# Optimization experiments

Hardware: AMD Instinct MI355X
Metric: run time of the kernel (lower is better)

Reference implementation:

```python
import jax, jax.numpy as jnp
import numpy as np

EPS = 1e-5


def _conv1x1(x, w, b):
    # x: (B,C,H,W), w: (O,C), b: (O,)
    return jnp.einsum('oc,bchw->bohw', w, x) + b[None, :, None, None]


def _attn(q, k, v):
    # q,k: (B,Dq,H,W); v: (B,C,H,W). Full NxN attention, softmax over keys.
    B, _, H, W = q.shape
    N = H * W
    Q = q.reshape(B, -1, N)
    K = k.reshape(B, -1, N)
    V = v.reshape(B, -1, N)
    A = jax.nn.softmax(jnp.einsum('bci,bcj->bij', Q, K), axis=-1)  # (B,N,N)
    out = jnp.einsum('bcj,bij->bci', V, A)  # out[b,c,i] = sum_j V[b,c,j] A[b,i,j]
    return out.reshape(B, -1, H, W)


def _std(feat):
    # torch.var(dim=2) is unbiased (ddof=1)
    B, C = feat.shape[:2]
    v = jnp.var(feat.reshape(B, C, -1), axis=2, ddof=1) + EPS
    return jnp.sqrt(v)[:, :, None, None]


def _fmm(fb_feat, bg_feat):
    return fb_feat * (_std(bg_feat) / _std(fb_feat))


def setup_inputs() -> dict:
    key = jax.random.key(0)
    ks = jax.random.split(key, 16)
    B, C, H, W = 2, 256, 64, 64
    D = C // 8
    s = 0.05
    inp = {
        'x': jax.random.normal(ks[0], (B, C, H, W), jnp.float32),
        'mask': jax.random.randint(ks[1], (B, 1, H, W), 0, 2).astype(jnp.float32),
        'sa_wq': jax.random.normal(ks[2], (D, C), jnp.float32) * s,
        'sa_bq': jax.random.normal(ks[3], (D,), jnp.float32) * s,
        'sa_wk': jax.random.normal(ks[4], (D, C), jnp.float32) * s,
        'sa_bk': jax.random.normal(ks[5], (D,), jnp.float32) * s,
        'sa_wv': jax.random.normal(ks[6], (C, C), jnp.float32) * s,
        'sa_bv': jax.random.normal(ks[7], (C,), jnp.float32) * s,
        'sa_gamma': jax.random.uniform(ks[8], (1,), jnp.float32),
        'wq': jax.random.normal(ks[9], (D, C), jnp.float32) * s,
        'bq': jax.random.normal(ks[10], (D,), jnp.float32) * s,
        'wk': jax.random.normal(ks[11], (D, C), jnp.float32) * s,
        'bk': jax.random.normal(ks[12], (D,), jnp.float32) * s,
        'wv': jax.random.normal(ks[13], (C, C), jnp.float32) * s,
        'bv': jax.random.normal(ks[14], (C,), jnp.float32) * s,
        'gamma': jax.random.uniform(ks[15], (1,), jnp.float32),
    }
    return inp


def reference(x, mask, sa_wq, sa_bq, sa_wk, sa_bk, sa_wv, sa_bv, sa_gamma,
              wq, bq, wk, bk, wv, bv, gamma):
    # --- Self_Attn ---
    sa_out = _attn(_conv1x1(x, sa_wq, sa_bq),
                   _conv1x1(x, sa_wk, sa_bk),
                   _conv1x1(x, sa_wv, sa_bv))
    x = sa_gamma[0] * sa_out + x
    # --- FB_FMM masked cross attention (mask already at feature resolution) ---
    reverse_mask = 1.0 - mask
    feature_b = reverse_mask * x
    feature_f = mask * x
    sw_bg = _attn(_conv1x1(feature_f, wq, bq),
                  _conv1x1(feature_b, wk, bk),
                  _conv1x1(feature_b, wv, bv))
    out = x + gamma[0] * _fmm(feature_f, sw_bg)
    return out
```

## Files before the change

### kernel.cpp

```cpp
#include <hip/hip_runtime.h>
#include <stdint.h>

typedef _Float16 f16;
typedef __attribute__((ext_vector_type(8))) _Float16 half8;
typedef __attribute__((ext_vector_type(2))) __fp16 fp16x2;
typedef __attribute__((ext_vector_type(8))) short short8;
typedef __attribute__((ext_vector_type(4))) float f32x4;

#define NPOS 4096
#define CCH  256
#define OQK  64
#define BATCH 2
#define NSPLIT 4
#define KEYS_PER_SPLIT 1024
#define NT (KEYS_PER_SPLIT / 64)

typedef __attribute__((address_space(3))) uint32_t lds_u32;
typedef __attribute__((address_space(1))) const uint32_t glb_u32;

__device__ __forceinline__ float bf2f(short u) {
    union { uint32_t i; float f; } c;
    c.i = ((uint32_t)(uint16_t)u) << 16;
    return c.f;
}
__device__ __forceinline__ short f2bf(float f) {
    union { float f; uint32_t i; } c; c.f = f;
    uint32_t lsb = (c.i >> 16) & 1u;
    c.i += 0x7FFFu + lsb;
    return (short)(c.i >> 16);
}

__device__ __forceinline__ bool detect_bf16(const uint32_t* mw) {
    int hits = 0;
    #pragma unroll
    for (int i = 0; i < 64; ++i) hits += ((mw[i] & 0xFFFFu) == 0x3F80u) ? 1 : 0;
    return hits != 0;
}

__device__ __forceinline__ void load8(const void* base, size_t e0, bool bf, float* v) {
    if (bf) {
        short8 s = *(const short8*)((const short*)base + e0);
        #pragma unroll
        for (int j = 0; j < 8; ++j) v[j] = bf2f(s[j]);
    } else {
        const float* fp = (const float*)base + e0;
        float4 a = *(const float4*)fp;
        float4 b = *(const float4*)(fp + 4);
        v[0] = a.x; v[1] = a.y; v[2] = a.z; v[3] = a.w;
        v[4] = b.x; v[5] = b.y; v[6] = b.z; v[7] = b.w;
    }
}
__device__ __forceinline__ float load1(const void* base, int i, bool bf) {
    return bf ? bf2f(((const short*)base)[i]) : ((const float*)base)[i];
}

__device__ __forceinline__ int pkrtz(float a, float b) {
    union { fp16x2 h; int i; } u;
    u.h = __builtin_amdgcn_cvt_pkrtz(a, b);
    return u.i;
}

__global__ __launch_bounds__(256) void convert_inputs(
    const uint32_t* __restrict__ mask_raw,
    const void* __restrict__ w1q, const void* __restrict__ w1k, const void* __restrict__ w1v_,
    const void* __restrict__ b1q, const void* __restrict__ b1k, const void* __restrict__ b1v_,
    const void* __restrict__ g1,
    const void* __restrict__ w2q, const void* __restrict__ w2k, const void* __restrict__ w2v_,
    const void* __restrict__ b2q, const void* __restrict__ b2k, const void* __restrict__ b2v_,
    const void* __restrict__ g2,
    float* __restrict__ maskf,
    f16* __restrict__ w1qk, f16* __restrict__ w1vm, f16* __restrict__ b1,
    f16* __restrict__ w2qk, f16* __restrict__ w2vm, f16* __restrict__ b2,
    float* __restrict__ gam)
{
    const bool bf = detect_bf16(mask_raw);
    const int blk = blockIdx.x, tid = threadIdx.x;
    float v[8];
    if (blk < 4) {
        const size_t e0 = ((size_t)blk * 256 + tid) * 8;
        load8(mask_raw, e0, bf, v);
        float4 f0 = {v[0], v[1], v[2], v[3]}, f1 = {v[4], v[5], v[6], v[7]};
        *(float4*)(maskf + e0) = f0;
        *(float4*)(maskf + e0 + 4) = f1;
    } else if (blk < 12) {
        const size_t g = ((size_t)(blk - 4) * 256 + tid) * 8;
        const int o = (int)(g >> 8), cc = (int)(g & 255);
        const void* src = (o < 32) ? w1q : w1k;
        const size_t se = (size_t)((o < 32) ? o : o - 32) * 256 + cc;
        load8(src, se, bf, v);
        half8 h;
        #pragma unroll
        for (int j = 0; j < 8; ++j) h[j] = (f16)v[j];
        *(half8*)(w1qk + g) = h;
    } else if (blk < 44) {
        const size_t g = ((size_t)(blk - 12) * 256 + tid) * 8;
        load8(w1v_, g, bf, v);
        half8 h;
        #pragma unroll
        for (int j = 0; j < 8; ++j) h[j] = (f16)v[j];
        *(half8*)(w1vm + g) = h;
    } else if (blk < 52) {
        const size_t g = ((size_t)(blk - 44) * 256 + tid) * 8;
        const int o = (int)(g >> 8), cc = (int)(g & 255);
        const void* src = (o < 32) ? w2q : w2k;
        const size_t se = (size_t)((o < 32) ? o : o - 32) * 256 + cc;
        load8(src, se, bf, v);
        half8 h;
        #pragma unroll
        for (int j = 0; j < 8; ++j) h[j] = (f16)v[j];
        *(half8*)(w2qk + g) = h;
    } else if (blk < 84) {
        const size_t g = ((size_t)(blk - 52) * 256 + tid) * 8;
        load8(w2v_, g, bf, v);
        half8 h;
        #pragma unroll
        for (int j = 0; j < 8; ++j) h[j] = (f16)v[j];
        *(half8*)(w2vm + g) = h;
    } else {
        for (int i = tid; i < 320; i += 256) {
            const void* s1 = (i < 32) ? b1q : (i < 64) ? b1k : b1v_;
            const void* s2 = (i < 32) ? b2q : (i < 64) ? b2k : b2v_;
            const int ii = (i < 32) ? i : (i < 64) ? i - 32 : i - 64;
            b1[i] = (f16)load1(s1, ii, bf);
            b2[i] = (f16)load1(s2, ii, bf);
        }
        if (tid == 0) {
            gam[0] = load1(g1, 0, bf);
            gam[1] = load1(g2, 0, bf);
        }
    }
}

__global__ __launch_bounds__(256) void conv_qkv(
    const void* __restrict__ xin, int is_raw,
    const uint32_t* __restrict__ mask_raw,
    const f16* __restrict__ wqk,
    const f16* __restrict__ wvm,
    const f16* __restrict__ bias,
    const float* __restrict__ maskf, int use_mask,
    f16* __restrict__ qkout,
    f16* __restrict__ vout)
{
    const bool bf = is_raw ? detect_bf16(mask_raw) : false;
    const int b    = blockIdx.y;
    const int n0   = blockIdx.x * 32;
    const int tid  = threadIdx.x;
    const int lane = tid & 63;
    const int w    = tid >> 6;
    const int lo   = lane & 15;
    const int hi   = lane >> 4;

    __shared__ f16 xt[32 * 256];

    {
        const int nc = tid & 3;
        const int cg = tid >> 2;
        #pragma unroll
        for (int it = 0; it < 4; ++it) {
            const int c = cg + 64 * it;
            const size_t off = ((size_t)b * CCH + c) * NPOS + n0 + nc * 8;
            float v8[8];
            load8(xin, off, bf, v8);
            #pragma unroll
            for (int j = 0; j < 8; ++j) {
                const int n = nc * 8 + j;
                int byte = n * 512 + c * 2;
                byte ^= ((n & 7) << 4);
                *(f16*)((char*)xt + byte) = (f16)v8[j];
            }
        }
    }
    __syncthreads();

    const f32x4 z = {0.f, 0.f, 0.f, 0.f};
    f32x4 acc_qk[2];
    f32x4 acc_v[4][2];
    #pragma unroll
    for (int i = 0; i < 2; ++i) {
        acc_qk[i] = z;
        #pragma unroll
        for (int j = 0; j < 4; ++j) acc_v[j][i] = z;
    }

    #pragma unroll 1
    for (int ks = 0; ks < 8; ++ks) {
        const int ce = ks * 32 + 8 * hi;
        half8 xfr[2];
        #pragma unroll
        for (int nt = 0; nt < 2; ++nt) {
            const int n = nt * 16 + lo;
            int byte = n * 512 + ce * 2;
            byte ^= ((n & 7) << 4);
            xfr[nt] = *(const half8*)((const char*)xt + byte);
        }
        {
            half8 wf = *(const half8*)(wqk + (size_t)(w * 16 + lo) * 256 + ce);
            #pragma unroll
            for (int nt = 0; nt < 2; ++nt)
                acc_qk[nt] = __builtin_amdgcn_mfma_f32_16x16x32_f16(xfr[nt], wf, acc_qk[nt], 0, 0, 0);
        }
        #pragma unroll
        for (int ot = 0; ot < 4; ++ot) {
            half8 wf = *(const half8*)(wvm + (size_t)(w * 64 + ot * 16 + lo) * 256 + ce);
            #pragma unroll
            for (int nt = 0; nt < 2; ++nt)
                acc_v[ot][nt] = __builtin_amdgcn_mfma_f32_16x16x32_f16(wf, xfr[nt], acc_v[ot][nt], 0, 0, 0);
        }
    }

    {
        const int o = w * 16 + lo;
        const float bb = (float)bias[o];
        #pragma unroll
        for (int nt = 0; nt < 2; ++nt) {
            #pragma unroll
            for (int r = 0; r < 4; ++r) {
                const int n = n0 + nt * 16 + 4 * hi + r;
                float mult = 1.f;
                if (use_mask) {
                    const float mv = maskf[b * NPOS + n];
                    mult = (o < 32) ? mv : (1.f - mv);
                }
                qkout[((size_t)b * NPOS + n) * OQK + o] = (f16)(mult * acc_qk[nt][r] + bb);
            }
        }
    }
    {
        float mv_n[2];
        #pragma unroll
        for (int nt = 0; nt < 2; ++nt)
            mv_n[nt] = use_mask ? (1.f - maskf[b * NPOS + n0 + nt * 16 + lo]) : 1.f;
        #pragma unroll
        for (int ot = 0; ot < 4; ++ot) {
            #pragma unroll
            for (int r = 0; r < 4; ++r) {
                const int oc = w * 64 + ot * 16 + 4 * hi + r;
                const float bb = (float)bias[64 + oc];
                #pragma unroll
                for (int nt = 0; nt < 2; ++nt) {
                    const int n = n0 + nt * 16 + lo;
                    vout[((size_t)b * CCH + oc) * NPOS + n] = (f16)(mv_n[nt] * acc_v[ot][nt][r] + bb);
                }
            }
        }
    }
}

__global__ __launch_bounds__(256, 2) void attn_split(
    const f16* __restrict__ qk,
    const f16* __restrict__ vbuf,
    f16* __restrict__ po,
    float2* __restrict__ pml)
{
    const int b     = blockIdx.z;
    const int split = blockIdx.y;
    const int tid   = threadIdx.x;
    const int lane  = tid & 63;
    const int w     = tid >> 6;
    const int lo    = lane & 15;
    const int hi    = lane >> 4;
    const int q0    = blockIdx.x * 64;
    const int qown  = w * 16;
    const int qA    = (w >> 1) * 32;
    const int qB    = qA + 16;
    const int cbase = (w & 1) * 128;

    __shared__ f16 kv[CCH * 64];
    __shared__ f16 kbuf[2][64 * 64];
    __shared__ f16 plds[64 * 72];
    __shared__ float sc_lds[64];
    __shared__ float l_lds[64];
    __shared__ int   flag_lds[4];

    const int trow = tid >> 3;
    const int tch  = tid & 7;

    const half8 qfrag = *(const half8*)(qk + ((size_t)b * NPOS + q0 + qown + lo) * OQK + 8 * hi);

    const f32x4 z = {0.f, 0.f, 0.f, 0.f};
    f32x4 accA[8], accB[8];
    #pragma unroll
    for (int i = 0; i < 8; ++i) { accA[i] = z; accB[i] = z; }
    float m_run = -3.0e38f, l_run = 0.f;

    const f16* vsrc = vbuf + (size_t)b * CCH * NPOS;
    const f16* ksrc = qk + (size_t)b * NPOS * OQK;

    #define STAGE_K(kt)                                                        \
    {                                                                          \
        const int j0s = split * KEYS_PER_SPLIT + (kt) * 64;                    \
        char* kb = (char*)kbuf + ((kt) & 1) * 8192;                            \
        _Pragma("unroll")                                                      \
        for (int i = 0; i < 2; ++i) {                                          \
            const int j = i * 32 + trow;                                       \
            const f16* g = ksrc + (size_t)(j0s + j) * OQK + ((tch ^ (j & 7)) * 8); \
            char* d = kb + i * 4096 + w * 1024;                                \
            __builtin_amdgcn_global_load_lds((glb_u32*)g, (lds_u32*)d, 16, 0, 0); \
        }                                                                      \
    }
    #define STAGE_V(kt)                                                        \
    {                                                                          \
        const int j0s = split * KEYS_PER_SPLIT + (kt) * 64;                    \
        _Pragma("unroll")                                                      \
        for (int i = 0; i < 8; ++i) {                                          \
            const int c = i * 32 + trow;                                       \
            const f16* g = vsrc + (size_t)c * NPOS + j0s + ((tch ^ (c & 7)) * 8); \
            char* d = (char*)kv + i * 4096 + w * 1024;                         \
            __builtin_amdgcn_global_load_lds((glb_u32*)g, (lds_u32*)d, 16, 0, 0); \
        }                                                                      \
    }

    STAGE_K(0)
    STAGE_V(0)

    #pragma unroll 1
    for (int kt = 0; kt < NT; ++kt) {
        asm volatile("s_waitcnt vmcnt(8)" ::: "memory");
        __builtin_amdgcn_s_barrier();
        asm volatile("" ::: "memory");
        if (kt + 1 < NT) STAGE_K(kt + 1)

        const char* kb = (const char*)kbuf + (kt & 1) * 8192;
        f32x4 s[4];
        __builtin_amdgcn_s_setprio(1);
        #pragma unroll
        for (int jt = 0; jt < 4; ++jt) {
            const int krow = jt * 16 + lo;
            const half8 kfrag = *(const half8*)(kb + krow * 128
                                                + ((64 + hi * 16) ^ ((krow & 7) << 4)));
            s[jt] = __builtin_amdgcn_mfma_f32_16x16x32_f16(kfrag, qfrag, z, 0, 0, 0);
        }
        __builtin_amdgcn_s_setprio(0);
        float pm = s[0][0];
        #pragma unroll
        for (int jt = 0; jt < 4; ++jt)
            #pragma unroll
            for (int r = 0; r < 4; ++r) pm = fmaxf(pm, s[jt][r]);
        pm = fmaxf(pm, __shfl_xor(pm, 16, 64));
        pm = fmaxf(pm, __shfl_xor(pm, 32, 64));
        const bool g = __any(pm - m_run > 8.f);
        float scv = 1.f;
        if (g) {
            const float mnew = fmaxf(m_run, pm);
            scv = __expf(m_run - mnew);
            m_run = mnew;
            l_run *= scv;
        }
        float rs = 0.f;
        #pragma unroll
        for (int jt = 0; jt < 4; ++jt) {
            #pragma unroll
            for (int r = 0; r < 4; ++r) {
                const float pv = __expf(s[jt][r] - m_run);
                s[jt][r] = pv;
                rs += pv;
            }
        }
        rs += __shfl_xor(rs, 16, 64);
        rs += __shfl_xor(rs, 32, 64);
        l_run += rs;
        #pragma unroll
        for (int jt = 0; jt < 4; ++jt) {
            union { int i2[2]; uint64_t u; } pw;
            pw.i2[0] = pkrtz(s[jt][0], s[jt][1]);
            pw.i2[1] = pkrtz(s[jt][2], s[jt][3]);
            *(uint64_t*)((char*)plds + (qown + lo) * 144 + jt * 32 + 8 * hi) = pw.u;
        }
        if (hi == 0) sc_lds[qown + lo] = scv;
        if (lane == 0) flag_lds[w] = g ? 1 : 0;

        asm volatile("s_waitcnt lgkmcnt(0)" ::: "memory");
        if (kt + 1 < NT) {
            asm volatile("s_waitcnt vmcnt(2)" ::: "memory");
        } else {
            asm volatile("s_waitcnt vmcnt(0)" ::: "memory");
        }
        __builtin_amdgcn_s_barrier();
        asm volatile("" ::: "memory");

        const int fA = flag_lds[(w >> 1) * 2];
        const int fB = flag_lds[(w >> 1) * 2 + 1];
        if (fA) {
            const float sa = sc_lds[qA + lo];
            #pragma unroll
            for (int ct = 0; ct < 8; ++ct) accA[ct] *= sa;
        }
        if (fB) {
            const float sb = sc_lds[qB + lo];
            #pragma unroll
            for (int ct = 0; ct < 8; ++ct) accB[ct] *= sb;
        }
        __builtin_amdgcn_s_setprio(1);
        #pragma unroll
        for (int ksp = 0; ksp < 2; ++ksp) {
            const half8 pfA = *(const half8*)((const char*)plds + (qA + lo) * 144 + ksp * 64 + 16 * hi);
            const half8 pfB = *(const half8*)((const char*)plds + (qB + lo) * 144 + ksp * 64 + 16 * hi);
            #pragma unroll
            for (int ct = 0; ct < 8; ++ct) {
                const int vrow = cbase + ct * 16 + lo;
                const half8 vfrag = *(const half8*)((const char*)kv + vrow * 128
                                                    + ((ksp * 64 + hi * 16) ^ ((vrow & 7) << 4)));
                accA[ct] = __builtin_amdgcn_mfma_f32_16x16x32_f16(vfrag, pfA, accA[ct], 0, 0, 0);
                accB[ct] = __builtin_amdgcn_mfma_f32_16x16x32_f16(vfrag, pfB, accB[ct], 0, 0, 0);
            }
        }
        __builtin_amdgcn_s_setprio(0);
        asm volatile("" ::: "memory");
        __builtin_amdgcn_s_barrier();
        asm volatile("" ::: "memory");
        if (kt + 1 < NT) STAGE_V(kt + 1)
    }
    #undef STAGE_K
    #undef STAGE_V

    if (hi == 0) {
        l_lds[qown + lo] = l_run;
        float2 v; v.x = m_run; v.y = l_run;
        pml[((size_t)split * BATCH + b) * NPOS + q0 + qown + lo] = v;
    }
    __syncthreads();
    const float invA = 1.f / l_lds[qA + lo];
    const float invB = 1.f / l_lds[qB + lo];
    f16* pob = po + (((size_t)split * BATCH + b) * CCH + cbase) * NPOS + q0;
    #pragma unroll
    for (int ct = 0; ct < 8; ++ct) {
        #pragma unroll
        for (int r = 0; r < 4; ++r) {
            const size_t rowo = (size_t)(ct * 16 + 4 * hi + r) * NPOS;
            pob[rowo + qA + lo] = (f16)(accA[ct][r] * invA);
            pob[rowo + qB + lo] = (f16)(accB[ct][r] * invB);
        }
    }
}

__global__ __launch_bounds__(256) void attn_merge(
    const f16* __restrict__ po,
    const float2* __restrict__ pml,
    const void* __restrict__ xraw,
    const uint32_t* __restrict__ mask_raw,
    const float* __restrict__ gamp,
    float* __restrict__ out_f,
    f16* __restrict__ out_h,
    int add_residual)
{
    const int b  = blockIdx.z;
    const int n0 = blockIdx.x * 64;
    const int c0 = blockIdx.y * 32;
    const int tid = threadIdx.x;
    const int cl  = tid >> 3;
    const int oct = tid & 7;

    __shared__ float wls[NSPLIT][64];
    if (tid < 64) {
        const int n = n0 + tid;
        float m[NSPLIT], l[NSPLIT];
        #pragma unroll
        for (int s = 0; s < NSPLIT; ++s) {
            float2 v = pml[((size_t)s * BATCH + b) * NPOS + n];
            m[s] = v.x; l[s] = v.y;
        }
        float M = m[0];
        #pragma unroll
        for (int s = 1; s < NSPLIT; ++s) M = fmaxf(M, m[s]);
        float wgt[NSPLIT], wsum = 0.f;
        #pragma unroll
        for (int s = 0; s < NSPLIT; ++s) { wgt[s] = __expf(m[s] - M) * l[s]; wsum += wgt[s]; }
        const float winv = 1.f / wsum;
        #pragma unroll
        for (int s = 0; s < NSPLIT; ++s) wls[s][tid] = wgt[s] * winv;
    }
    __syncthreads();

    const int c = c0 + cl;
    const int nl = oct * 8;
    const size_t base = ((size_t)b * CCH + c) * NPOS + n0 + nl;
    float o[8] = {0.f, 0.f, 0.f, 0.f, 0.f, 0.f, 0.f, 0.f};
    #pragma unroll
    for (int s = 0; s < NSPLIT; ++s) {
        const half8 pv = *(const half8*)(po + (((size_t)s * BATCH + b) * CCH + c) * NPOS + n0 + nl);
        const float* wr = &wls[s][nl];
        #pragma unroll
        for (int j = 0; j < 8; ++j) o[j] += wr[j] * (float)pv[j];
    }
    if (add_residual) {
        const bool bf = detect_bf16(mask_raw);
        const float gamma = gamp[0];
        float xv[8];
        load8(xraw, base, bf, xv);
        float4 f0, f1;
        f0.x = gamma * o[0] + xv[0]; f0.y = gamma * o[1] + xv[1];
        f0.z = gamma * o[2] + xv[2]; f0.w = gamma * o[3] + xv[3];
        f1.x = gamma * o[4] + xv[4]; f1.y = gamma * o[5] + xv[5];
        f1.z = gamma * o[6] + xv[6]; f1.w = gamma * o[7] + xv[7];
        *(float4*)(out_f + base) = f0;
        *(float4*)(out_f + base + 4) = f1;
    } else {
        half8 h;
        #pragma unroll
        for (int j = 0; j < 8; ++j) h[j] = (f16)o[j];
        *(half8*)(out_h + base) = h;
    }
}

__global__ __launch_bounds__(256) void fmm_final(
    const float* __restrict__ x1f,
    const f16*  __restrict__ bg,
    const float* __restrict__ maskf,
    const float* __restrict__ gamp,
    const uint32_t* __restrict__ mask_raw,
    void* __restrict__ outp)
{
    const bool bf = detect_bf16(mask_raw);
    const int b = blockIdx.y;
    const int c = blockIdx.x;
    const int tid = threadIdx.x;
    const size_t rowoff = ((size_t)b * CCH + c) * NPOS;
    const float* xrow = x1f + rowoff;
    const f16*  grow = bg + rowoff;
    const float* mrow = maskf + (size_t)b * NPOS;

    float s_f = 0.f, ss_f = 0.f, s_g = 0.f, ss_g = 0.f;
    #pragma unroll
    for (int u = 0; u < 2; ++u) {
        const int i = tid * 16 + u * 8;
        const float4 x0 = *(const float4*)(xrow + i);
        const float4 x1v = *(const float4*)(xrow + i + 4);
        const float4 m0 = *(const float4*)(mrow + i);
        const float4 m1 = *(const float4*)(mrow + i + 4);
        half8 gv = *(const half8*)(grow + i);
        const float xs[8] = {x0.x, x0.y, x0.z, x0.w, x1v.x, x1v.y, x1v.z, x1v.w};
        const float ms[8] = {m0.x, m0.y, m0.z, m0.w, m1.x, m1.y, m1.z, m1.w};
        #pragma unroll
        for (int j = 0; j < 8; ++j) {
            const float f = xs[j] * ms[j];
            const float g = (float)gv[j];
            s_f += f; ss_f += f * f;
            s_g += g; ss_g += g * g;
        }
    }
    #pragma unroll
    for (int off = 1; off < 64; off <<= 1) {
        s_f += __shfl_xor(s_f, off, 64);
        ss_f += __shfl_xor(ss_f, off, 64);
        s_g += __shfl_xor(s_g, off, 64);
        ss_g += __shfl_xor(ss_g, off, 64);
    }
    __shared__ float red[4][4];
    const int wv_ = tid >> 6;
    if ((tid & 63) == 0) {
        red[wv_][0] = s_f; red[wv_][1] = ss_f; red[wv_][2] = s_g; red[wv_][3] = ss_g;
    }
    __syncthreads();
    s_f  = red[0][0] + red[1][0] + red[2][0] + red[3][0];
    ss_f = red[0][1] + red[1][1] + red[2][1] + red[3][1];
    s_g  = red[0][2] + red[1][2] + red[2][2] + red[3][2];
    ss_g = red[0][3] + red[1][3] + red[2][3] + red[3][3];

    const float nn = 4096.f, nm1 = 4095.f;
    const float var_f = (ss_f - s_f * s_f / nn) / nm1;
    const float var_g = (ss_g - s_g * s_g / nn) / nm1;
    const float ratio = sqrtf((var_g + 1e-5f) / (var_f + 1e-5f));
    const float gamma = gamp[0];

    #pragma unroll
    for (int u = 0; u < 2; ++u) {
        const int i = tid * 16 + u * 8;
        const float4 x0 = *(const float4*)(xrow + i);
        const float4 x1v = *(const float4*)(xrow + i + 4);
        const float4 m0 = *(const float4*)(mrow + i);
        const float4 m1 = *(const float4*)(mrow + i + 4);
        const float xs[8] = {x0.x, x0.y, x0.z, x0.w, x1v.x, x1v.y, x1v.z, x1v.w};
        const float ms[8] = {m0.x, m0.y, m0.z, m0.w, m1.x, m1.y, m1.z, m1.w};
        float ov[8];
        #pragma unroll
        for (int j = 0; j < 8; ++j)
            ov[j] = xs[j] + gamma * (xs[j] * ms[j]) * ratio;
        if (bf) {
            short8 sv;
            #pragma unroll
            for (int j = 0; j < 8; ++j) sv[j] = f2bf(ov[j]);
            *(short8*)((short*)outp + rowoff + i) = sv;
        } else {
            float4 f0 = {ov[0], ov[1], ov[2], ov[3]}, f1 = {ov[4], ov[5], ov[6], ov[7]};
            *(float4*)((float*)outp + rowoff + i) = f0;
            *(float4*)((float*)outp + rowoff + i + 4) = f1;
        }
    }
}

extern "C" void kernel_launch(void* const* d_in, const int* in_sizes, int n_in,
                              void* d_out, int out_size, void* d_ws, size_t ws_size,
                              hipStream_t stream)
{
    const size_t MB = 1u << 20, KB = 1u << 10;
    char* ws = (char*)d_ws;
    f16*    qkbuf = (f16*)(ws);
    f16*    vbuf  = (f16*)(ws + 1 * MB);
    f16*    bgbuf = (f16*)(ws);
    float*  x1f   = (float*)(ws + 5 * MB);
    f16*    po    = (f16*)(ws + 13 * MB);
    float2* pml   = (float2*)(ws + 29 * MB);
    float*  maskf = (float*)(ws + 29 * MB + 512 * KB);
    f16*    w1qk  = (f16*)(ws + 30 * MB);
    f16*    w1v   = (f16*)(ws + 30 * MB + 32 * KB);
    f16*    b1    = (f16*)(ws + 30 * MB + 160 * KB);
    f16*    w2qk  = (f16*)(ws + 30 * MB + 164 * KB);
    f16*    w2v   = (f16*)(ws + 30 * MB + 196 * KB);
    f16*    b2    = (f16*)(ws + 30 * MB + 324 * KB);
    float*  gam   = (float*)(ws + 30 * MB + 328 * KB);

    const uint32_t* mraw = (const uint32_t*)d_in[1];

    dim3 blk(256);
    dim3 vgrid(85);
    dim3 cgrid(NPOS / 32, BATCH);
    dim3 agrid(NPOS / 64, NSPLIT, BATCH);
    dim3 mgrid(NPOS / 64, CCH / 32, BATCH);
    dim3 fgrid(CCH, BATCH);

    convert_inputs<<<vgrid, blk, 0, stream>>>(
        mraw,
        d_in[2], d_in[4], d_in[6], d_in[3], d_in[5], d_in[7], d_in[8],
        d_in[9], d_in[11], d_in[13], d_in[10], d_in[12], d_in[14], d_in[15],
        maskf, w1qk, w1v, b1, w2qk, w2v, b2, gam);

    conv_qkv<<<cgrid, blk, 0, stream>>>(d_in[0], 1, mraw, w1qk, w1v, b1, maskf, 0, qkbuf, vbuf);
    attn_split<<<agrid, blk, 0, stream>>>(qkbuf, vbuf, po, pml);
    attn_merge<<<mgrid, blk, 0, stream>>>(po, pml, d_in[0], mraw, gam + 0, x1f, nullptr, 1);
    conv_qkv<<<cgrid, blk, 0, stream>>>(x1f, 0, mraw, w2qk, w2v, b2, maskf, 1, qkbuf, vbuf);
    attn_split<<<agrid, blk, 0, stream>>>(qkbuf, vbuf, po, pml);
    attn_merge<<<mgrid, blk, 0, stream>>>(po, pml, nullptr, mraw, gam + 1, nullptr, bgbuf, 0);
    fmm_final<<<fgrid, blk, 0, stream>>>(x1f, bgbuf, maskf, gam + 1, mraw, d_out);
}
```

Measured before the change: 125.1 us.

## Use 512-thread attention blocks with split QK/PV wave roles and deeper K prefetch

The split attention kernel moves from 256 to 512 threads per block. Four waves compute QK scores and the softmax, and all eight waves share the PV MFMA work, each owning 32 V channels across all 64 queries. K tiles are now prefetched two iterations ahead. The P tile in LDS drops its padding and uses an XOR swizzle instead. The aim is more waves per CU to hide latency and smaller per-wave accumulators, at the cost of idle waves during the softmax phase and a stricter vmcnt(0) wait at the end of each iteration.

```diff
diff --git a/kernel.cpp b/kernel.cpp
--- a/kernel.cpp
+++ b/kernel.cpp
@@ -246,7 +246,7 @@
     }
 }
 
-__global__ __launch_bounds__(256, 2) void attn_split(
+__global__ __launch_bounds__(512, 4) void attn_split(
     const f16* __restrict__ qk,
     const f16* __restrict__ vbuf,
     f16* __restrict__ po,
@@ -260,14 +260,12 @@
     const int lo    = lane & 15;
     const int hi    = lane >> 4;
     const int q0    = blockIdx.x * 64;
-    const int qown  = w * 16;
-    const int qA    = (w >> 1) * 32;
-    const int qB    = qA + 16;
-    const int cbase = (w & 1) * 128;
+    const int qown  = (w & 3) * 16;
+    const int cbase = w * 32;
 
     __shared__ f16 kv[CCH * 64];
     __shared__ f16 kbuf[2][64 * 64];
-    __shared__ f16 plds[64 * 72];
+    __shared__ f16 plds[64 * 64];
     __shared__ float sc_lds[64];
     __shared__ float l_lds[64];
     __shared__ int   flag_lds[4];
@@ -275,160 +273,167 @@
     const int trow = tid >> 3;
     const int tch  = tid & 7;
 
-    const half8 qfrag = *(const half8*)(qk + ((size_t)b * NPOS + q0 + qown + lo) * OQK + 8 * hi);
+    half8 qfrag;
+    if (w < 4)
+        qfrag = *(const half8*)(qk + ((size_t)b * NPOS + q0 + qown + lo) * OQK + 8 * hi);
 
     const f32x4 z = {0.f, 0.f, 0.f, 0.f};
-    f32x4 accA[8], accB[8];
-    #pragma unroll
-    for (int i = 0; i < 8; ++i) { accA[i] = z; accB[i] = z; }
+    f32x4 acc[2][4];
+    #pragma unroll
+    for (int i = 0; i < 2; ++i)
+        #pragma unroll
+        for (int j = 0; j < 4; ++j) acc[i][j] = z;
     float m_run = -3.0e38f, l_run = 0.f;
 
     const f16* vsrc = vbuf + (size_t)b * CCH * NPOS;
     const f16* ksrc = qk + (size_t)b * NPOS * OQK;
 
+    #define STAGE_V(kt)                                                        \
+    {                                                                          \
+        const int j0s = split * KEYS_PER_SPLIT + (kt) * 64;                    \
+        _Pragma("unroll")                                                      \
+        for (int i = 0; i < 4; ++i) {                                          \
+            const int c = i * 64 + trow;                                       \
+            const f16* g = vsrc + (size_t)c * NPOS + j0s + ((tch ^ (c & 7)) * 8); \
+            char* d = (char*)kv + i * 8192 + w * 1024;                         \
+            __builtin_amdgcn_global_load_lds((glb_u32*)g, (lds_u32*)d, 16, 0, 0); \
+        }                                                                      \
+    }
     #define STAGE_K(kt)                                                        \
     {                                                                          \
         const int j0s = split * KEYS_PER_SPLIT + (kt) * 64;                    \
         char* kb = (char*)kbuf + ((kt) & 1) * 8192;                            \
-        _Pragma("unroll")                                                      \
-        for (int i = 0; i < 2; ++i) {                                          \
-            const int j = i * 32 + trow;                                       \
-            const f16* g = ksrc + (size_t)(j0s + j) * OQK + ((tch ^ (j & 7)) * 8); \
-            char* d = kb + i * 4096 + w * 1024;                                \
-            __builtin_amdgcn_global_load_lds((glb_u32*)g, (lds_u32*)d, 16, 0, 0); \
-        }                                                                      \
-    }
-    #define STAGE_V(kt)                                                        \
-    {                                                                          \
-        const int j0s = split * KEYS_PER_SPLIT + (kt) * 64;                    \
-        _Pragma("unroll")                                                      \
-        for (int i = 0; i < 8; ++i) {                                          \
-            const int c = i * 32 + trow;                                       \
-            const f16* g = vsrc + (size_t)c * NPOS + j0s + ((tch ^ (c & 7)) * 8); \
-            char* d = (char*)kv + i * 4096 + w * 1024;                         \
-            __builtin_amdgcn_global_load_lds((glb_u32*)g, (lds_u32*)d, 16, 0, 0); \
-        }                                                                      \
-    }
-
+        const f16* g = ksrc + (size_t)(j0s + trow) * OQK + ((tch ^ (trow & 7)) * 8); \
+        __builtin_amdgcn_global_load_lds((glb_u32*)g, (lds_u32*)(kb + w * 1024), 16, 0, 0); \
+    }
+
+    STAGE_V(0)
     STAGE_K(0)
-    STAGE_V(0)
+    STAGE_K(1)
+    asm volatile("s_waitcnt vmcnt(1)" ::: "memory");
+    __builtin_amdgcn_s_barrier();
+    asm volatile("" ::: "memory");
 
     #pragma unroll 1
     for (int kt = 0; kt < NT; ++kt) {
-        asm volatile("s_waitcnt vmcnt(8)" ::: "memory");
+        if (w < 4) {
+            const char* kb = (const char*)kbuf + (kt & 1) * 8192;
+            f32x4 s[4];
+            __builtin_amdgcn_s_setprio(1);
+            #pragma unroll
+            for (int jt = 0; jt < 4; ++jt) {
+                const int krow = jt * 16 + lo;
+                const half8 kfrag = *(const half8*)(kb + krow * 128
+                                                    + ((64 + hi * 16) ^ ((krow & 7) << 4)));
+                s[jt] = __builtin_amdgcn_mfma_f32_16x16x32_f16(kfrag, qfrag, z, 0, 0, 0);
+            }
+            __builtin_amdgcn_s_setprio(0);
+            float pm = s[0][0];
+            #pragma unroll
+            for (int jt = 0; jt < 4; ++jt)
+                #pragma unroll
+                for (int r = 0; r < 4; ++r) pm = fmaxf(pm, s[jt][r]);
+            pm = fmaxf(pm, __shfl_xor(pm, 16, 64));
+            pm = fmaxf(pm, __shfl_xor(pm, 32, 64));
+            const bool g = __any(pm - m_run > 8.f);
+            float scv = 1.f;
+            if (g) {
+                const float mnew = fmaxf(m_run, pm);
+                scv = __expf(m_run - mnew);
+                m_run = mnew;
+                l_run *= scv;
+            }
+            float rs = 0.f;
+            #pragma unroll
+            for (int jt = 0; jt < 4; ++jt) {
+                #pragma unroll
+                for (int r = 0; r < 4; ++r) {
+                    const float pv = __expf(s[jt][r] - m_run);
+                    s[jt][r] = pv;
+                    rs += pv;
+                }
+            }
+            rs += __shfl_xor(rs, 16, 64);
+            rs += __shfl_xor(rs, 32, 64);
+            l_run += rs;
+            const int q = qown + lo;
+            #pragma unroll
+            for (int jt = 0; jt < 4; ++jt) {
+                union { int i2[2]; uint64_t u; } pw;
+                pw.i2[0] = pkrtz(s[jt][0], s[jt][1]);
+                pw.i2[1] = pkrtz(s[jt][2], s[jt][3]);
+                *(uint64_t*)((char*)plds + q * 128 + ((jt * 32 + 8 * hi) ^ ((q & 7) << 4))) = pw.u;
+            }
+            if (hi == 0) sc_lds[q] = scv;
+            if (lane == 0) flag_lds[w] = g ? 1 : 0;
+        }
+
+        asm volatile("s_waitcnt lgkmcnt(0)" ::: "memory");
+        if (kt + 1 < NT) {
+            asm volatile("s_waitcnt vmcnt(1)" ::: "memory");
+        } else {
+            asm volatile("s_waitcnt vmcnt(0)" ::: "memory");
+        }
+        __builtin_amdgcn_sched_barrier(0);
         __builtin_amdgcn_s_barrier();
         asm volatile("" ::: "memory");
-        if (kt + 1 < NT) STAGE_K(kt + 1)
-
-        const char* kb = (const char*)kbuf + (kt & 1) * 8192;
-        f32x4 s[4];
+
+        #pragma unroll
+        for (int qt = 0; qt < 4; ++qt) {
+            if (flag_lds[qt]) {
+                const float sc = sc_lds[qt * 16 + lo];
+                #pragma unroll
+                for (int ct = 0; ct < 2; ++ct) acc[ct][qt] *= sc;
+            }
+        }
         __builtin_amdgcn_s_setprio(1);
         #pragma unroll
-        for (int jt = 0; jt < 4; ++jt) {
-            const int krow = jt * 16 + lo;
-            const half8 kfrag = *(const half8*)(kb + krow * 128
-                                                + ((64 + hi * 16) ^ ((krow & 7) << 4)));
-            s[jt] = __builtin_amdgcn_mfma_f32_16x16x32_f16(kfrag, qfrag, z, 0, 0, 0);
+        for (int ksp = 0; ksp < 2; ++ksp) {
+            half8 pf[4];
+            #pragma unroll
+            for (int qt = 0; qt < 4; ++qt)
+                pf[qt] = *(const half8*)((const char*)plds + (qt * 16 + lo) * 128
+                                         + ((ksp * 64 + 16 * hi) ^ ((lo & 7) << 4)));
+            #pragma unroll
+            for (int ct = 0; ct < 2; ++ct) {
+                const int vrow = cbase + ct * 16 + lo;
+                const half8 vf = *(const half8*)((const char*)kv + vrow * 128
+                                                 + ((ksp * 64 + 16 * hi) ^ ((vrow & 7) << 4)));
+                #pragma unroll
+                for (int qt = 0; qt < 4; ++qt)
+                    acc[ct][qt] = __builtin_amdgcn_mfma_f32_16x16x32_f16(vf, pf[qt], acc[ct][qt], 0, 0, 0);
+            }
         }
         __builtin_amdgcn_s_setprio(0);
-        float pm = s[0][0];
-        #pragma unroll
-        for (int jt = 0; jt < 4; ++jt)
-            #pragma unroll
-            for (int r = 0; r < 4; ++r) pm = fmaxf(pm, s[jt][r]);
-        pm = fmaxf(pm, __shfl_xor(pm, 16, 64));
-        pm = fmaxf(pm, __shfl_xor(pm, 32, 64));
-        const bool g = __any(pm - m_run > 8.f);
-        float scv = 1.f;
-        if (g) {
-            const float mnew = fmaxf(m_run, pm);
-            scv = __expf(m_run - mnew);
-            m_run = mnew;
-            l_run *= scv;
-        }
-        float rs = 0.f;
-        #pragma unroll
-        for (int jt = 0; jt < 4; ++jt) {
-            #pragma unroll
-            for (int r = 0; r < 4; ++r) {
-                const float pv = __expf(s[jt][r] - m_run);
-                s[jt][r] = pv;
-                rs += pv;
-            }
-        }
-        rs += __shfl_xor(rs, 16, 64);
-        rs += __shfl_xor(rs, 32, 64);
-        l_run += rs;
-        #pragma unroll
-        for (int jt = 0; jt < 4; ++jt) {
-            union { int i2[2]; uint64_t u; } pw;
-            pw.i2[0] = pkrtz(s[jt][0], s[jt][1]);
-            pw.i2[1] = pkrtz(s[jt][2], s[jt][3]);
-            *(uint64_t*)((char*)plds + (qown + lo) * 144 + jt * 32 + 8 * hi) = pw.u;
-        }
-        if (hi == 0) sc_lds[qown + lo] = scv;
-        if (lane == 0) flag_lds[w] = g ? 1 : 0;
-
-        asm volatile("s_waitcnt lgkmcnt(0)" ::: "memory");
-        if (kt + 1 < NT) {
-            asm volatile("s_waitcnt vmcnt(2)" ::: "memory");
-        } else {
-            asm volatile("s_waitcnt vmcnt(0)" ::: "memory");
-        }
-        __builtin_amdgcn_s_barrier();
-        asm volatile("" ::: "memory");
-
-        const int fA = flag_lds[(w >> 1) * 2];
-        const int fB = flag_lds[(w >> 1) * 2 + 1];
-        if (fA) {
-            const float sa = sc_lds[qA + lo];
-            #pragma unroll
-            for (int ct = 0; ct < 8; ++ct) accA[ct] *= sa;
-        }
-        if (fB) {
-            const float sb = sc_lds[qB + lo];
-            #pragma unroll
-            for (int ct = 0; ct < 8; ++ct) accB[ct] *= sb;
-        }
-        __builtin_amdgcn_s_setprio(1);
-        #pragma unroll
-        for (int ksp = 0; ksp < 2; ++ksp) {
-            const half8 pfA = *(const half8*)((const char*)plds + (qA + lo) * 144 + ksp * 64 + 16 * hi);
-            const half8 pfB = *(const half8*)((const char*)plds + (qB + lo) * 144 + ksp * 64 + 16 * hi);
-            #pragma unroll
-            for (int ct = 0; ct < 8; ++ct) {
-                const int vrow = cbase + ct * 16 + lo;
-                const half8 vfrag = *(const half8*)((const char*)kv + vrow * 128
-                                                    + ((ksp * 64 + hi * 16) ^ ((vrow & 7) << 4)));
-                accA[ct] = __builtin_amdgcn_mfma_f32_16x16x32_f16(vfrag, pfA, accA[ct], 0, 0, 0);
-                accB[ct] = __builtin_amdgcn_mfma_f32_16x16x32_f16(vfrag, pfB, accB[ct], 0, 0, 0);
-            }
-        }
-        __builtin_amdgcn_s_setprio(0);
-        asm volatile("" ::: "memory");
+
+        asm volatile("s_waitcnt lgkmcnt(0) vmcnt(0)" ::: "memory");
+        __builtin_amdgcn_sched_barrier(0);
         __builtin_amdgcn_s_barrier();
         asm volatile("" ::: "memory");
         if (kt + 1 < NT) STAGE_V(kt + 1)
+        if (kt + 2 < NT) STAGE_K(kt + 2)
     }
     #undef STAGE_K
     #undef STAGE_V
 
-    if (hi == 0) {
+    if (w < 4 && hi == 0) {
         l_lds[qown + lo] = l_run;
         float2 v; v.x = m_run; v.y = l_run;
         pml[((size_t)split * BATCH + b) * NPOS + q0 + qown + lo] = v;
     }
     __syncthreads();
-    const float invA = 1.f / l_lds[qA + lo];
-    const float invB = 1.f / l_lds[qB + lo];
+    float inv[4];
+    #pragma unroll
+    for (int qt = 0; qt < 4; ++qt) inv[qt] = 1.f / l_lds[qt * 16 + lo];
     f16* pob = po + (((size_t)split * BATCH + b) * CCH + cbase) * NPOS + q0;
     #pragma unroll
-    for (int ct = 0; ct < 8; ++ct) {
+    for (int ct = 0; ct < 2; ++ct) {
         #pragma unroll
         for (int r = 0; r < 4; ++r) {
             const size_t rowo = (size_t)(ct * 16 + 4 * hi + r) * NPOS;
-            pob[rowo + qA + lo] = (f16)(accA[ct][r] * invA);
-            pob[rowo + qB + lo] = (f16)(accB[ct][r] * invB);
+            #pragma unroll
+            for (int qt = 0; qt < 4; ++qt)
+                pob[rowo + qt * 16 + lo] = (f16)(acc[ct][qt][r] * inv[qt]);
         }
     }
 }
@@ -612,6 +617,7 @@
     const uint32_t* mraw = (const uint32_t*)d_in[1];
 
     dim3 blk(256);
+    dim3 ablk(512);
     dim3 vgrid(85);
     dim3 cgrid(NPOS / 32, BATCH);
     dim3 agrid(NPOS / 64, NSPLIT, BATCH);
@@ -625,10 +631,10 @@
         maskf, w1qk, w1v, b1, w2qk, w2v, b2, gam);
 
     conv_qkv<<<cgrid, blk, 0, stream>>>(d_in[0], 1, mraw, w1qk, w1v, b1, maskf, 0, qkbuf, vbuf);
-    attn_split<<<agrid, blk, 0, stream>>>(qkbuf, vbuf, po, pml);
+    attn_split<<<agrid, ablk, 0, stream>>>(qkbuf, vbuf, po, pml);
     attn_merge<<<mgrid, blk, 0, stream>>>(po, pml, d_in[0], mraw, gam + 0, x1f, nullptr, 1);
     conv_qkv<<<cgrid, blk, 0, stream>>>(x1f, 0, mraw, w2qk, w2v, b2, maskf, 1, qkbuf, vbuf);
-    attn_split<<<agrid, blk, 0, stream>>>(qkbuf, vbuf, po, pml);
+    attn_split<<<agrid, ablk, 0, stream>>>(qkbuf, vbuf, po, pml);
     attn_merge<<<mgrid, blk, 0, stream>>>(po, pml, nullptr, mraw, gam + 1, nullptr, bgbuf, 0);
     fmm_final<<<fgrid, blk, 0, stream>>>(x1f, bgbuf, maskf, gam + 1, mraw, d_out);
 }
```

New measurement: 123.9 us. Within noise of the previous version (-0.9%).
